# Kernel optimization log

Hardware: AMD Instinct MI355X
Metric: run time of the kernel (lower is better)

The kernel has to match this reference:

```python
import jax, jax.numpy as jnp
import numpy as np

N = 100_000          # nodes
E = 1_600_000        # edges (avg degree 16)
LRELU = 0.01         # default nn.LeakyReLU slope (MLP / bottleneck)
SLOPE = 0.2          # GAT attention slope


def leaky(x, s):
    return jnp.where(x >= 0, x, s * x)


def dense_block(x, convW, gamma, beta):
    # x: [N, C0]; convW: [L, G, Cmax]; each layer: BN -> LeakyReLU -> 1x1 conv -> concat
    for i in range(convW.shape[0]):
        c = x.shape[1]                       # static under trace
        mu = x.mean(axis=0)
        var = x.var(axis=0)                  # biased var, matches torch BN train mode
        xn = (x - mu) * jax.lax.rsqrt(var + 1e-5) * gamma[i, :c] + beta[i, :c]
        xn = leaky(xn, LRELU)
        x = jnp.concatenate([x, xn @ convW[i, :, :c].T], axis=1)  # [N, c+G]
    return x


def gat(x, W, a, b, src, dst):
    # single effective head (torch code shares weight/a across heads -> identical heads)
    h = x @ W                                # [N, F]
    F = W.shape[1]
    # per-edge logit: LeakyReLU([h_dst || h_src] @ a)
    e = leaky(h[dst] @ a[:F] + h[src] @ a[F:], SLOPE)   # [E]
    m = jax.ops.segment_max(e, dst, num_segments=N)
    m = jnp.where(jnp.isfinite(m), m, 0.0)
    ex = jnp.exp(e - m[dst])
    den = jax.ops.segment_sum(ex, dst, num_segments=N)
    alpha = ex / (den[dst] + 1e-16)
    out = jax.ops.segment_sum(alpha[:, None] * h[src], dst, num_segments=N)
    return out + b


def setup_inputs() -> dict:
    key = jax.random.key(0)
    ks = jax.random.split(key, 16)

    def w(k, shape, fan_in):
        return jax.random.normal(k, shape, jnp.float32) / np.float32(np.sqrt(fan_in))

    return {
        "x": jax.random.normal(ks[0], (N, 64), jnp.float32),
        "src": jax.random.randint(ks[1], (E,), 0, N, jnp.int64 if jax.config.jax_enable_x64 else jnp.int32),
        "dst": jax.random.randint(ks[2], (E,), 0, N, jnp.int64 if jax.config.jax_enable_x64 else jnp.int32),
        "mlp_w1": w(ks[3], (64, 256), 64),
        "mlp_b1": jnp.zeros((256,), jnp.float32),
        "mlp_w2": w(ks[4], (256, 256), 256),
        "mlp_b2": jnp.zeros((256,), jnp.float32),
        "mlp_w3": w(ks[5], (256, 24), 256),
        "mlp_b3": jnp.zeros((24,), jnp.float32),
        "conv1": w(ks[6], (6, 12, 84), 84),
        "bn1_g": jnp.ones((6, 84), jnp.float32),
        "bn1_b": jnp.zeros((6, 84), jnp.float32),
        "gat1_w": w(ks[7], (96, 48), 96),
        "gat1_a": jax.random.normal(ks[8], (96,), jnp.float32) * 0.1,
        "gat1_b": jnp.zeros((48,), jnp.float32),
        "conv2": w(ks[9], (6, 12, 108), 108),
        "bn2_g": jnp.ones((6, 108), jnp.float32),
        "bn2_b": jnp.zeros((6, 108), jnp.float32),
        "gat2_w": w(ks[10], (120, 60), 120),
        "gat2_a": jax.random.normal(ks[11], (120,), jnp.float32) * 0.1,
        "gat2_b": jnp.zeros((60,), jnp.float32),
        "conv3": w(ks[12], (6, 12, 120), 120),
        "bn3_g": jnp.ones((6, 120), jnp.float32),
        "bn3_b": jnp.zeros((6, 120), jnp.float32),
    }


def reference(x, src, dst,
              mlp_w1, mlp_b1, mlp_w2, mlp_b2, mlp_w3, mlp_b3,
              conv1, bn1_g, bn1_b, gat1_w, gat1_a, gat1_b,
              conv2, bn2_g, bn2_b, gat2_w, gat2_a, gat2_b,
              conv3, bn3_g, bn3_b):
    h = leaky(x @ mlp_w1 + mlp_b1, LRELU)
    h = leaky(h @ mlp_w2 + mlp_b2, LRELU)
    h = leaky(h @ mlp_w3 + mlp_b3, LRELU)          # [N, 24]
    h = dense_block(h, conv1, bn1_g, bn1_b)        # [N, 96]
    h = gat(h, gat1_w, gat1_a, gat1_b, src, dst)   # [N, 48]
    h = dense_block(h, conv2, bn2_g, bn2_b)        # [N, 120]
    h = gat(h, gat2_w, gat2_a, gat2_b, src, dst)   # [N, 60]
    h = dense_block(h, conv3, bn3_g, bn3_b)        # [N, 132]
    return h
```

## Files before the change

### kernel.cpp

```cpp
#include <hip/hip_runtime.h>
#include <math.h>

#define N_NODES 100000
#define N_EDGES 1600000

static constexpr int GG = (N_NODES + 63) / 64;
static constexpr int NODE_GRID = (N_NODES + 255) / 256;
static constexpr int NB = (N_NODES + 255) / 256;

typedef __attribute__((ext_vector_type(8))) short          bf16x8;
typedef __attribute__((ext_vector_type(8))) unsigned short ushort8_t;
typedef __attribute__((ext_vector_type(4))) unsigned short ushort4_t;
typedef __attribute__((ext_vector_type(4))) float          f32x4;

__device__ __forceinline__ float lrelu(float v, float s){ return v >= 0.f ? v : v*s; }

__device__ __forceinline__ unsigned short f2bf(float f){
    unsigned u = __float_as_uint(f);
    unsigned r = (u + 0x7FFFu + ((u >> 16) & 1u)) >> 16;
    return (unsigned short)r;
}
__device__ __forceinline__ float bf2f(unsigned short h){
    return __uint_as_float(((unsigned)h) << 16);
}

__global__ void cvt_wT_split(const float* __restrict__ w,
                             unsigned short* __restrict__ whi,
                             unsigned short* __restrict__ wlo,
                             int K, int Nsrc, int Npad)
{
    int idx = blockIdx.x * 256 + threadIdx.x;
    if (idx >= Npad * K) return;
    int n = idx / K, k = idx % K;
    float v = (n < Nsrc) ? w[(long)k * Nsrc + n] : 0.f;
    unsigned short hi = f2bf(v);
    whi[idx] = hi;
    wlo[idx] = f2bf(v - bf2f(hi));
}

template<int KV>
__global__ __launch_bounds__(256) void mlp_mfma_hilo(
    const float* __restrict__ A,
    const unsigned short* __restrict__ wth, const unsigned short* __restrict__ wtl,
    const float* __restrict__ bias, float* __restrict__ Out)
{
    constexpr int AS = KV + 8;
    __shared__ unsigned short lds_hi[64 * AS];
    __shared__ unsigned short lds_lo[64 * AS];
    const int t = threadIdx.x;
    const int r0 = blockIdx.x * 64;
    const int wv = t >> 6, lane = t & 63;
    const int l15 = lane & 15, grp = lane >> 4;
    const int cw = wv * 64;

    constexpr int cpr = KV / 8;
    for (int c = t; c < 64 * cpr; c += 256) {
        int row = c / cpr, kc = c % cpr;
        int gr = r0 + row;
        float4 v0 = make_float4(0,0,0,0), v1 = v0;
        if (gr < N_NODES) {
            v0 = *(const float4*)(A + (long)gr * KV + kc * 8);
            v1 = *(const float4*)(A + (long)gr * KV + kc * 8 + 4);
        }
        float vs[8] = {v0.x,v0.y,v0.z,v0.w,v1.x,v1.y,v1.z,v1.w};
        unsigned short* ph = lds_hi + row * AS + kc * 8;
        unsigned short* pl = lds_lo + row * AS + kc * 8;
#pragma unroll
        for (int j = 0; j < 8; j++) {
            unsigned short hi = f2bf(vs[j]);
            ph[j] = hi;
            pl[j] = f2bf(vs[j] - bf2f(hi));
        }
    }
    __syncthreads();

    f32x4 acc[4][4];
#pragma unroll
    for (int i = 0; i < 4; i++)
#pragma unroll
        for (int j = 0; j < 4; j++) acc[i][j] = (f32x4){0.f,0.f,0.f,0.f};

#pragma unroll
    for (int ks = 0; ks < KV / 32; ks++) {
        bf16x8 ah[4], al[4], bh[4], bl[4];
#pragma unroll
        for (int i = 0; i < 4; i++) {
            ah[i] = *(const bf16x8*)(lds_hi + (i*16 + l15) * AS + ks*32 + grp*8);
            al[i] = *(const bf16x8*)(lds_lo + (i*16 + l15) * AS + ks*32 + grp*8);
        }
#pragma unroll
        for (int j = 0; j < 4; j++) {
            bh[j] = *(const bf16x8*)(wth + (size_t)(cw + j*16 + l15) * KV + ks*32 + grp*8);
            bl[j] = *(const bf16x8*)(wtl + (size_t)(cw + j*16 + l15) * KV + ks*32 + grp*8);
        }
#pragma unroll
        for (int i = 0; i < 4; i++)
#pragma unroll
            for (int j = 0; j < 4; j++) {
                acc[i][j] = __builtin_amdgcn_mfma_f32_16x16x32_bf16(ah[i], bl[j], acc[i][j], 0, 0, 0);
                acc[i][j] = __builtin_amdgcn_mfma_f32_16x16x32_bf16(al[i], bh[j], acc[i][j], 0, 0, 0);
                acc[i][j] = __builtin_amdgcn_mfma_f32_16x16x32_bf16(ah[i], bh[j], acc[i][j], 0, 0, 0);
            }
    }

    __syncthreads();
#pragma unroll
    for (int i = 0; i < 4; i++)
#pragma unroll
        for (int j = 0; j < 4; j++)
#pragma unroll
            for (int r = 0; r < 4; r++) {
                int row = r0 + i*16 + grp*4 + r;
                int col = cw + j*16 + l15;
                if (row < N_NODES) {
                    float v = acc[i][j][r] + bias[col];
                    Out[(long)row * 256 + col] = lrelu(v, 0.01f);
                }
            }
}

__global__ __launch_bounds__(256) void mlp_mfma24_hilo(
    const float* __restrict__ A,
    const unsigned short* __restrict__ wth, const unsigned short* __restrict__ wtl,
    const float* __restrict__ bias, float* __restrict__ XtOut)
{
    constexpr int KV = 256, AS = 264;
    __shared__ unsigned short lds_hi[64 * AS];
    __shared__ unsigned short lds_lo[64 * AS];
    const int t = threadIdx.x;
    const int r0 = blockIdx.x * 64;
    const int wv = t >> 6, lane = t & 63;
    const int l15 = lane & 15, grp = lane >> 4;

    constexpr int cpr = KV / 8;
    for (int c = t; c < 64 * cpr; c += 256) {
        int row = c / cpr, kc = c % cpr;
        int gr = r0 + row;
        float4 v0 = make_float4(0,0,0,0), v1 = v0;
        if (gr < N_NODES) {
            v0 = *(const float4*)(A + (long)gr * KV + kc * 8);
            v1 = *(const float4*)(A + (long)gr * KV + kc * 8 + 4);
        }
        float vs[8] = {v0.x,v0.y,v0.z,v0.w,v1.x,v1.y,v1.z,v1.w};
        unsigned short* ph = lds_hi + row * AS + kc * 8;
        unsigned short* pl = lds_lo + row * AS + kc * 8;
#pragma unroll
        for (int j = 0; j < 8; j++) {
            unsigned short hi = f2bf(vs[j]);
            ph[j] = hi;
            pl[j] = f2bf(vs[j] - bf2f(hi));
        }
    }
    __syncthreads();

    f32x4 acc[2] = {(f32x4){0.f,0.f,0.f,0.f}, (f32x4){0.f,0.f,0.f,0.f}};
#pragma unroll
    for (int ks = 0; ks < KV / 32; ks++) {
        bf16x8 ah = *(const bf16x8*)(lds_hi + (wv*16 + l15) * AS + ks*32 + grp*8);
        bf16x8 al = *(const bf16x8*)(lds_lo + (wv*16 + l15) * AS + ks*32 + grp*8);
#pragma unroll
        for (int j = 0; j < 2; j++) {
            bf16x8 bh = *(const bf16x8*)(wth + (size_t)(j*16 + l15) * KV + ks*32 + grp*8);
            bf16x8 bl = *(const bf16x8*)(wtl + (size_t)(j*16 + l15) * KV + ks*32 + grp*8);
            acc[j] = __builtin_amdgcn_mfma_f32_16x16x32_bf16(ah, bl, acc[j], 0, 0, 0);
            acc[j] = __builtin_amdgcn_mfma_f32_16x16x32_bf16(al, bh, acc[j], 0, 0, 0);
            acc[j] = __builtin_amdgcn_mfma_f32_16x16x32_bf16(ah, bh, acc[j], 0, 0, 0);
        }
    }

    __syncthreads();
    float* ldsf = (float*)lds_hi;
#pragma unroll
    for (int j = 0; j < 2; j++)
#pragma unroll
        for (int r = 0; r < 4; r++) {
            int cl = j*16 + l15;
            if (cl < 24) {
                int rl = wv*16 + grp*4 + r;
                float v = acc[j][r] + bias[cl];
                ldsf[rl * 25 + cl] = lrelu(v, 0.01f);
            }
        }
    __syncthreads();
    int n = t & 63, c0 = t >> 6;
    int gr = r0 + n;
    if (gr < N_NODES)
        for (int c = c0; c < 24; c += 4)
            XtOut[(long)c * N_NODES + gr] = ldsf[n * 25 + c];
}

__global__ void bn_stats_t(const float* __restrict__ Xt,
                           float* __restrict__ gsum, float* __restrict__ gsq)
{
    int ch = blockIdx.x, part = blockIdx.y, t = threadIdx.x;
    const float* p = Xt + (long)ch * N_NODES;
    float s = 0.f, q = 0.f;
    for (long i = (long)part * 25000 + t * 4; i < (long)(part + 1) * 25000; i += 1024) {
        float4 v = *(const float4*)(p + i);
        s += v.x + v.y + v.z + v.w;
        q += v.x*v.x + v.y*v.y + v.z*v.z + v.w*v.w;
    }
#pragma unroll
    for (int m = 1; m < 64; m <<= 1) {
        s += __shfl_xor(s, m, 64);
        q += __shfl_xor(q, m, 64);
    }
    __shared__ float ls[4], lq[4];
    int wid = t >> 6;
    if ((t & 63) == 0) { ls[wid] = s; lq[wid] = q; }
    __syncthreads();
    if (t == 0) {
        atomicAdd(gsum + ch, ls[0] + ls[1] + ls[2] + ls[3]);
        atomicAdd(gsq  + ch, lq[0] + lq[1] + lq[2] + lq[3]);
    }
}

__global__ __launch_bounds__(256) void dense_conv2(
    float* __restrict__ Xt, int C, int C0, int layerIdx,
    const float* __restrict__ W, int WS,
    const float* __restrict__ gamma, const float* __restrict__ beta,
    const float* __restrict__ gsum, const float* __restrict__ gsq,
    float* __restrict__ psq)
{
    constexpr int QOFF = 6 * 12 * NB;
    __shared__ float w_lds[12 * 132];
    __shared__ float a_lds[132], b_lds[132];
    __shared__ float red[2][4][12];
    const int t = threadIdx.x;

    for (int c = t; c < C; c += 256) {
        float s, q;
        if (c < C0) { s = gsum[c]; q = gsq[c]; }
        else {
            int lc = c - C0;
            int lj = lc / 12, g = lc % 12;
            const float* pp = psq + ((size_t)lj * 12 + g) * NB;
            const float* qq = pp + QOFF;
            s = 0.f; q = 0.f;
            for (int b = 0; b < NB; b++) { s += pp[b]; q += qq[b]; }
        }
        float mu  = s * (1.f / N_NODES);
        float var = q * (1.f / N_NODES) - mu * mu;
        float A = rsqrtf(var + 1e-5f) * gamma[c];
        a_lds[c] = A;
        b_lds[c] = beta[c] - mu * A;
    }
    for (int i = t; i < 12 * C; i += 256) {
        int g = i / C, c = i - g * C;
        w_lds[g * 132 + c] = W[g * WS + c];
    }
    __syncthreads();

    long n = (long)blockIdx.x * 256 + t;
    bool valid = (n < N_NODES);
    const float* xp = Xt + (valid ? n : 0);
    float acc[12];
#pragma unroll
    for (int g = 0; g < 12; g++) acc[g] = 0.f;

    float v[12], vn[12];
#pragma unroll
    for (int j = 0; j < 12; j++) v[j] = xp[(long)j * N_NODES];
    for (int c0 = 0; c0 < C; c0 += 12) {
        if (c0 + 12 < C) {
#pragma unroll
            for (int j = 0; j < 12; j++)
                vn[j] = xp[(long)(c0 + 12 + j) * N_NODES];
        }
#pragma unroll
        for (int j = 0; j < 12; j++) {
            int ch = c0 + j;
            float u = a_lds[ch] * v[j] + b_lds[ch];
            u = (u >= 0.f) ? u : 0.01f * u;
#pragma unroll
            for (int g = 0; g < 12; g++)
                acc[g] += u * w_lds[g * 132 + ch];
        }
#pragma unroll
        for (int j = 0; j < 12; j++) v[j] = vn[j];
    }
    if (valid) {
#pragma unroll
        for (int g = 0; g < 12; g++)
            Xt[(long)(C + g) * N_NODES + n] = acc[g];
    }

    if (layerIdx < 5) {
        float sv[12], qv[12];
#pragma unroll
        for (int g = 0; g < 12; g++) {
            float a = valid ? acc[g] : 0.f;
            sv[g] = a; qv[g] = a * a;
        }
#pragma unroll
        for (int m = 1; m < 64; m <<= 1)
#pragma unroll
            for (int g = 0; g < 12; g++) {
                sv[g] += __shfl_xor(sv[g], m, 64);
                qv[g] += __shfl_xor(qv[g], m, 64);
            }
        int wid = t >> 6;
        if ((t & 63) == 0) {
#pragma unroll
            for (int g = 0; g < 12; g++) { red[0][wid][g] = sv[g]; red[1][wid][g] = qv[g]; }
        }
        __syncthreads();
        if (t < 12) {
            float s = red[0][0][t] + red[0][1][t] + red[0][2][t] + red[0][3][t];
            float q = red[1][0][t] + red[1][1][t] + red[1][2][t] + red[1][3][t];
            psq[((size_t)layerIdx * 12 + t) * NB + blockIdx.x] = s;
            psq[QOFF + ((size_t)layerIdx * 12 + t) * NB + blockIdx.x] = q;
        }
    }
}

template<int F>
__global__ __launch_bounds__(256) void gat_gemm(
    const float* __restrict__ A, const float* __restrict__ B,
    const float* __restrict__ avec, int K,
    unsigned short* __restrict__ Hb, float* __restrict__ sd, float* __restrict__ ss)
{
    __shared__ float At[16 * 68];
    __shared__ float Bt[16 * 64];
    __shared__ float ad[64], as_[64];
    const int t  = threadIdx.x;
    const int r0 = blockIdx.x * 64;
    const int tx = t & 15, ty = t >> 4;
    if (t < 64) {
        ad[t]  = (t < F) ? avec[t]     : 0.f;
        as_[t] = (t < F) ? avec[F + t] : 0.f;
    }

    float acc[4][4];
#pragma unroll
    for (int i = 0; i < 4; i++)
#pragma unroll
        for (int j = 0; j < 4; j++) acc[i][j] = 0.f;

    for (int k0 = 0; k0 < K; k0 += 16) {
        {
            int kk = t >> 4, rq = t & 15;
            float4 v = make_float4(0.f,0.f,0.f,0.f);
            if (k0 + kk < K)
                v = *(const float4*)(A + (long)(k0 + kk) * N_NODES + r0 + rq * 4);
            *(float4*)(At + kk * 68 + rq * 4) = v;
        }
        for (int i = t; i < 16 * 64; i += 256) {
            int kk = i >> 6, mq = i & 63;
            float v = 0.f;
            if (k0 + kk < K && mq < F) v = B[(long)(k0 + kk) * F + mq];
            Bt[kk * 64 + mq] = v;
        }
        __syncthreads();
#pragma unroll
        for (int kk = 0; kk < 16; kk++) {
            float4 av = *(const float4*)(At + kk * 68 + ty * 4);
            float4 bv = *(const float4*)(Bt + kk * 64 + tx * 4);
            float a_[4] = {av.x, av.y, av.z, av.w};
            float b_[4] = {bv.x, bv.y, bv.z, bv.w};
#pragma unroll
            for (int i = 0; i < 4; i++)
#pragma unroll
                for (int j = 0; j < 4; j++)
                    acc[i][j] += a_[i] * b_[j];
        }
        __syncthreads();
    }

#pragma unroll
    for (int i = 0; i < 4; i++) {
        int row = r0 + ty * 4 + i;
        float pd = 0.f, pq_ = 0.f;
#pragma unroll
        for (int j = 0; j < 4; j++) {
            int col = tx * 4 + j;
            pd  += acc[i][j] * ad[col];
            pq_ += acc[i][j] * as_[col];
        }
#pragma unroll
        for (int m = 1; m < 16; m <<= 1) {
            pd  += __shfl_xor(pd,  m, 64);
            pq_ += __shfl_xor(pq_, m, 64);
        }
        if (row < N_NODES) {
            if (tx == 0) { sd[row] = pd; ss[row] = pq_; }
            if (tx * 4 < F) {
                ushort4_t u;
#pragma unroll
                for (int j = 0; j < 4; j++) u[j] = f2bf(acc[i][j]);
                *(ushort4_t*)(Hb + (long)row * 64 + tx * 4) = u;
            }
        }
    }
}

template<int F>
__global__ __launch_bounds__(256) void gat_aggregate2(
    const int* __restrict__ rstart, const int* __restrict__ csr_src,
    const float* __restrict__ sd, const float* __restrict__ ss,
    const unsigned short* __restrict__ Hb,
    const float* __restrict__ bias, float* __restrict__ outT)
{
    __shared__ float tile[64 * (F + 1)];
    const int t = threadIdx.x;
    const int wid = t >> 6, lane = t & 63;
    const long n0 = (long)blockIdx.x * 64;

#pragma unroll 1
    for (int k = 0; k < 16; k++) {
        long node = n0 + wid * 16 + k;
        float res = 0.f;
        if (node < N_NODES) {
            int st = rstart[node], en = rstart[node + 1];
            int deg = en - st;
            float sdn = sd[node];
            float acc = 0.f, dsum = 0.f;
            if (deg <= 64) {
                int sj = 0; float v = -3.4e38f;
                if (lane < deg) {
                    sj = csr_src[st + lane];
                    v = lrelu(sdn + ss[sj], 0.2f);
                }
                float m = v;
#pragma unroll
                for (int o = 1; o < 64; o <<= 1) m = fmaxf(m, __shfl_xor(m, o, 64));
                float p = (lane < deg) ? __expf(v - m) : 0.f;
                dsum = p;
                int j = 0;
                for (; j + 4 <= deg; j += 4) {
                    float a0 = __shfl(p, j, 64),   a1 = __shfl(p, j+1, 64);
                    float a2 = __shfl(p, j+2, 64), a3 = __shfl(p, j+3, 64);
                    int   s0 = __shfl(sj, j, 64),   s1 = __shfl(sj, j+1, 64);
                    int   s2 = __shfl(sj, j+2, 64), s3 = __shfl(sj, j+3, 64);
                    if (lane < F) {
                        float h0 = bf2f(Hb[(long)s0 * 64 + lane]);
                        float h1 = bf2f(Hb[(long)s1 * 64 + lane]);
                        float h2 = bf2f(Hb[(long)s2 * 64 + lane]);
                        float h3 = bf2f(Hb[(long)s3 * 64 + lane]);
                        acc += a0 * h0; acc += a1 * h1; acc += a2 * h2; acc += a3 * h3;
                    }
                }
                for (; j < deg; j++) {
                    float a = __shfl(p, j, 64);
                    int   s = __shfl(sj, j, 64);
                    if (lane < F) acc += a * bf2f(Hb[(long)s * 64 + lane]);
                }
            } else {
                float m = -3.4e38f;
                for (int base = st; base < en; base += 64) {
                    int cnt = min(64, en - base);
                    float v = -3.4e38f;
                    if (lane < cnt) {
                        int s = csr_src[base + lane];
                        v = lrelu(sdn + ss[s], 0.2f);
                    }
#pragma unroll
                    for (int o = 1; o < 64; o <<= 1) v = fmaxf(v, __shfl_xor(v, o, 64));
                    m = fmaxf(m, v);
                }
                for (int base = st; base < en; base += 64) {
                    int cnt = min(64, en - base);
                    float p = 0.f; int sj = 0;
                    if (lane < cnt) {
                        sj = csr_src[base + lane];
                        float v = lrelu(sdn + ss[sj], 0.2f);
                        p = __expf(v - m);
                    }
                    dsum += p;
                    int j = 0;
                    for (; j + 4 <= cnt; j += 4) {
                        float a0 = __shfl(p, j, 64),   a1 = __shfl(p, j+1, 64);
                        float a2 = __shfl(p, j+2, 64), a3 = __shfl(p, j+3, 64);
                        int   s0 = __shfl(sj, j, 64),   s1 = __shfl(sj, j+1, 64);
                        int   s2 = __shfl(sj, j+2, 64), s3 = __shfl(sj, j+3, 64);
                        if (lane < F) {
                            float h0 = bf2f(Hb[(long)s0 * 64 + lane]);
                            float h1 = bf2f(Hb[(long)s1 * 64 + lane]);
                            float h2 = bf2f(Hb[(long)s2 * 64 + lane]);
                            float h3 = bf2f(Hb[(long)s3 * 64 + lane]);
                            acc += a0 * h0; acc += a1 * h1; acc += a2 * h2; acc += a3 * h3;
                        }
                    }
                    for (; j < cnt; j++) {
                        float a = __shfl(p, j, 64);
                        int   s = __shfl(sj, j, 64);
                        if (lane < F) acc += a * bf2f(Hb[(long)s * 64 + lane]);
                    }
                }
            }
#pragma unroll
            for (int o = 1; o < 64; o <<= 1) dsum += __shfl_xor(dsum, o, 64);
            res = acc / (dsum + 1e-16f);
        }
        if (lane < F) tile[(wid * 16 + k) * (F + 1) + lane] = res + bias[lane];
    }
    __syncthreads();
    for (int idx = t; idx < F * 64; idx += 256) {
        int c = idx / 64, i = idx % 64;
        long n = n0 + i;
        if (n < N_NODES) outT[(long)c * N_NODES + n] = tile[i * (F + 1) + c];
    }
}

__global__ __launch_bounds__(256) void transpose_out(const float* __restrict__ Xt,
                                                     float* __restrict__ out)
{
    __shared__ float tile[64 * 133];
    int t = threadIdx.x;
    long n0 = (long)blockIdx.x * 64;
    int lane = t & 63, cq = t >> 6;
    for (int c = cq; c < 132; c += 4) {
        long n = n0 + lane;
        float v = (n < N_NODES) ? Xt[(long)c * N_NODES + n] : 0.f;
        tile[lane * 133 + c] = v;
    }
    __syncthreads();
    for (int idx = t; idx < 64 * 132; idx += 256) {
        int r = idx / 132, c = idx % 132;
        long n = n0 + r;
        if (n < N_NODES) out[n * 132 + c] = tile[r * 133 + c];
    }
}

__global__ void hist_kernel(const int* __restrict__ dst, int* __restrict__ deg)
{
    for (long e = (long)blockIdx.x * 256 + threadIdx.x; e < N_EDGES; e += (long)gridDim.x * 256)
        atomicAdd(deg + dst[e], 1);
}

__global__ void scan1(const int* __restrict__ deg, int* __restrict__ rtmp, int* __restrict__ parts)
{
    __shared__ int ls[256];
    int t = threadIdx.x;
    long i = (long)blockIdx.x * 256 + t;
    int v = (i < N_NODES) ? deg[i] : 0;
    ls[t] = v; __syncthreads();
    for (int o = 1; o < 256; o <<= 1) {
        int y = (t >= o) ? ls[t - o] : 0;
        __syncthreads();
        ls[t] += y;
        __syncthreads();
    }
    if (i < N_NODES) rtmp[i] = ls[t] - v;
    if (t == 255) parts[blockIdx.x] = ls[255];
}

__global__ void scan2(int* __restrict__ parts, int nb, int* __restrict__ total_out)
{
    __shared__ int ls[512];
    int t = threadIdx.x;
    int v = (t < nb) ? parts[t] : 0;
    ls[t] = v; __syncthreads();
    for (int o = 1; o < 512; o <<= 1) {
        int y = (t >= o) ? ls[t - o] : 0;
        __syncthreads();
        ls[t] += y;
        __syncthreads();
    }
    if (t < nb) parts[t] = ls[t] - v;
    if (t == 0) total_out[0] = ls[511];
}

__global__ void scan3(const int* __restrict__ rtmp, const int* __restrict__ parts,
                      int* __restrict__ rstart, int* __restrict__ cursor)
{
    long i = (long)blockIdx.x * 256 + threadIdx.x;
    if (i < N_NODES) {
        int v = rtmp[i] + parts[i >> 8];
        rstart[i] = v;
        cursor[i] = v;
    }
}

__global__ void scatter_k(const int* __restrict__ src, const int* __restrict__ dst,
                          int* __restrict__ cursor, int* __restrict__ csr_src)
{
    for (long e = (long)blockIdx.x * 256 + threadIdx.x; e < N_EDGES; e += (long)gridDim.x * 256) {
        int pos = atomicAdd(cursor + dst[e], 1);
        csr_src[pos] = src[e];
    }
}

static void run_dense_block_t(hipStream_t stream, float* Xt, int C0,
                              const float* convW, int WS,
                              const float* gamma, const float* beta,
                              float* gsum, float* gsq, float* psq)
{
    hipMemsetAsync(gsum, 0, 264 * sizeof(float), stream);
    bn_stats_t<<<dim3(C0, 4), 256, 0, stream>>>(Xt, gsum, gsq);
    for (int i = 0; i < 6; i++) {
        int C = C0 + 12 * i;
        dense_conv2<<<NB, 256, 0, stream>>>(Xt, C, C0, i, convW + (size_t)i * 12 * WS, WS,
                                            gamma + (size_t)i * WS, beta + (size_t)i * WS,
                                            gsum, gsq, psq);
    }
}

template<int F>
static void run_gat(hipStream_t stream, const float* XtIn, int K,
                    const float* W, const float* avec, const float* bias,
                    unsigned short* Hb, float* outT,
                    float* sd, float* ss, const int* rstart, const int* csr_src)
{
    gat_gemm<F><<<GG, 256, 0, stream>>>(XtIn, W, avec, K, Hb, sd, ss);
    gat_aggregate2<F><<<GG, 256, 0, stream>>>(rstart, csr_src, sd, ss, Hb, bias, outT);
}

extern "C" void kernel_launch(void* const* d_in, const int* in_sizes, int n_in,
                              void* d_out, int out_size, void* d_ws, size_t ws_size,
                              hipStream_t stream)
{
    const float* x     = (const float*)d_in[0];
    const int*   src   = (const int*)d_in[1];
    const int*   dst   = (const int*)d_in[2];
    const float* w1    = (const float*)d_in[3];
    const float* b1    = (const float*)d_in[4];
    const float* w2    = (const float*)d_in[5];
    const float* b2    = (const float*)d_in[6];
    const float* w3    = (const float*)d_in[7];
    const float* b3    = (const float*)d_in[8];
    const float* conv1 = (const float*)d_in[9];
    const float* bn1g  = (const float*)d_in[10];
    const float* bn1b  = (const float*)d_in[11];
    const float* g1w   = (const float*)d_in[12];
    const float* g1a   = (const float*)d_in[13];
    const float* g1b   = (const float*)d_in[14];
    const float* conv2 = (const float*)d_in[15];
    const float* bn2g  = (const float*)d_in[16];
    const float* bn2b  = (const float*)d_in[17];
    const float* g2w   = (const float*)d_in[18];
    const float* g2a   = (const float*)d_in[19];
    const float* g2b   = (const float*)d_in[20];
    const float* conv3 = (const float*)d_in[21];
    const float* bn3g  = (const float*)d_in[22];
    const float* bn3b  = (const float*)d_in[23];
    float* out = (float*)d_out;

    char* ws = (char*)d_ws;
    size_t off = 0;
    auto alloc = [&](size_t bytes) -> void* {
        void* p = ws + off;
        off += (bytes + 255) & ~(size_t)255;
        return p;
    };
    float*    h      = (float*)alloc((size_t)N_NODES * 256 * 4);
    float*    Xt1    = (float*)alloc((size_t)96  * N_NODES * 4);
    float*    Xt2    = (float*)alloc((size_t)120 * N_NODES * 4);
    int*      csr_src= (int*)alloc((size_t)N_EDGES * 4);
    int*      deg    = (int*)alloc((size_t)N_NODES * 4);
    int*      rtmp   = (int*)alloc((size_t)N_NODES * 4);
    int*      rstart = (int*)alloc((size_t)(N_NODES + 1) * 4);
    int*      cursor = (int*)alloc((size_t)N_NODES * 4);
    int*      parts  = (int*)alloc(2048);
    float*    sd     = (float*)alloc((size_t)N_NODES * 4);
    float*    ss     = (float*)alloc((size_t)N_NODES * 4);
    float*    gsum   = (float*)alloc(264 * 4);
    float*    gsq    = gsum + 132;
    float*    psq    = (float*)alloc((size_t)2 * 6 * 12 * NB * 4);
    unsigned short* wt1h = (unsigned short*)alloc(256 * 64  * 2);
    unsigned short* wt1l = (unsigned short*)alloc(256 * 64  * 2);
    unsigned short* wt2h = (unsigned short*)alloc(256 * 256 * 2);
    unsigned short* wt2l = (unsigned short*)alloc(256 * 256 * 2);
    unsigned short* wt3h = (unsigned short*)alloc(32  * 256 * 2);
    unsigned short* wt3l = (unsigned short*)alloc(32  * 256 * 2);

    unsigned short* Hb  = (unsigned short*)h;
    float* Xt3 = (float*)((char*)h + (size_t)16 * 1024 * 1024);

    hipMemsetAsync(deg, 0, (size_t)N_NODES * 4, stream);
    hist_kernel<<<2048, 256, 0, stream>>>(dst, deg);
    scan1<<<NODE_GRID, 256, 0, stream>>>(deg, rtmp, parts);
    scan2<<<1, 512, 0, stream>>>(parts, NODE_GRID, rstart + N_NODES);
    scan3<<<NODE_GRID, 256, 0, stream>>>(rtmp, parts, rstart, cursor);
    scatter_k<<<2048, 256, 0, stream>>>(src, dst, cursor, csr_src);

    cvt_wT_split<<<(256 * 64  + 255) / 256, 256, 0, stream>>>(w1, wt1h, wt1l, 64,  256, 256);
    cvt_wT_split<<<(256 * 256 + 255) / 256, 256, 0, stream>>>(w2, wt2h, wt2l, 256, 256, 256);
    cvt_wT_split<<<(32  * 256 + 255) / 256, 256, 0, stream>>>(w3, wt3h, wt3l, 256, 24,  32);

    mlp_mfma_hilo<64> <<<GG, 256, 0, stream>>>(x, wt1h, wt1l, b1, h);
    mlp_mfma_hilo<256><<<GG, 256, 0, stream>>>(h, wt2h, wt2l, b2, h);
    mlp_mfma24_hilo<<<GG, 256, 0, stream>>>(h, wt3h, wt3l, b3, Xt1);

    run_dense_block_t(stream, Xt1, 24, conv1, 84, bn1g, bn1b, gsum, gsq, psq);

    run_gat<48>(stream, Xt1, 96, g1w, g1a, g1b, Hb, Xt2, sd, ss, rstart, csr_src);

    run_dense_block_t(stream, Xt2, 48, conv2, 108, bn2g, bn2b, gsum, gsq, psq);

    run_gat<60>(stream, Xt2, 120, g2w, g2a, g2b, Hb, Xt3, sd, ss, rstart, csr_src);

    run_dense_block_t(stream, Xt3, 60, conv3, 120, bn3g, bn3b, gsum, gsq, psq);

    transpose_out<<<GG, 256, 0, stream>>>(Xt3, out);
}
```

Before: 1.152 ms.

## Build CSR via two-level bucket sort and wave-parallel BN partial reduction

Replaces the per-node histogram/scan/scatter CSR construction with a bucketed two-pass sort: edges are first binned by dst>>8 using LDS-local histograms and padded bucket counters, then each bucket is locally sorted in shared memory to emit rstart and csr_src. This is meant to cut global atomic contention on 100k per-node counters and the random scatter writes. It also changes the dense_conv2 prologue so each wavefront reduces a channel's per-block BN partials cooperatively with shuffles instead of one thread serially summing all blocks. The cost is an extra 8-byte pairs buffer pass, and edge order within a node becomes nondeterministic, which can alter floating-point summation order.

```diff
diff --git a/kernel.cpp b/kernel.cpp
--- a/kernel.cpp
+++ b/kernel.cpp
@@ -5,8 +5,8 @@
 #define N_EDGES 1600000
 
 static constexpr int GG = (N_NODES + 63) / 64;
-static constexpr int NODE_GRID = (N_NODES + 255) / 256;
 static constexpr int NB = (N_NODES + 255) / 256;
+static constexpr int NBKT = (N_NODES + 255) / 256;
 
 typedef __attribute__((ext_vector_type(8))) short          bf16x8;
 typedef __attribute__((ext_vector_type(8))) unsigned short ushort8_t;
@@ -227,24 +227,35 @@
     __shared__ float a_lds[132], b_lds[132];
     __shared__ float red[2][4][12];
     const int t = threadIdx.x;
-
-    for (int c = t; c < C; c += 256) {
-        float s, q;
-        if (c < C0) { s = gsum[c]; q = gsq[c]; }
-        else {
-            int lc = c - C0;
-            int lj = lc / 12, g = lc % 12;
-            const float* pp = psq + ((size_t)lj * 12 + g) * NB;
-            const float* qq = pp + QOFF;
-            s = 0.f; q = 0.f;
-            for (int b = 0; b < NB; b++) { s += pp[b]; q += qq[b]; }
-        }
+    const int wid = t >> 6, lane = t & 63;
+
+    for (int c = t; c < C0; c += 256) {
+        float s = gsum[c], q = gsq[c];
         float mu  = s * (1.f / N_NODES);
         float var = q * (1.f / N_NODES) - mu * mu;
         float A = rsqrtf(var + 1e-5f) * gamma[c];
         a_lds[c] = A;
         b_lds[c] = beta[c] - mu * A;
     }
+    for (int gc = wid; gc < C - C0; gc += 4) {
+        const float* pp = psq + (size_t)gc * NB;
+        const float* qq = psq + QOFF + (size_t)gc * NB;
+        float s = 0.f, q = 0.f;
+        for (int b = lane; b < NB; b += 64) { s += pp[b]; q += qq[b]; }
+#pragma unroll
+        for (int o = 1; o < 64; o <<= 1) {
+            s += __shfl_xor(s, o, 64);
+            q += __shfl_xor(q, o, 64);
+        }
+        if (lane == 0) {
+            int c = C0 + gc;
+            float mu  = s * (1.f / N_NODES);
+            float var = q * (1.f / N_NODES) - mu * mu;
+            float A = rsqrtf(var + 1e-5f) * gamma[c];
+            a_lds[c] = A;
+            b_lds[c] = beta[c] - mu * A;
+        }
+    }
     for (int i = t; i < 12 * C; i += 256) {
         int g = i / C, c = i - g * C;
         w_lds[g * 132 + c] = W[g * WS + c];
@@ -299,8 +310,7 @@
                 sv[g] += __shfl_xor(sv[g], m, 64);
                 qv[g] += __shfl_xor(qv[g], m, 64);
             }
-        int wid = t >> 6;
-        if ((t & 63) == 0) {
+        if (lane == 0) {
 #pragma unroll
             for (int g = 0; g < 12; g++) { red[0][wid][g] = sv[g]; red[1][wid][g] = qv[g]; }
         }
@@ -522,34 +532,25 @@
     }
 }
 
-__global__ void hist_kernel(const int* __restrict__ dst, int* __restrict__ deg)
-{
+__global__ __launch_bounds__(256) void bkt_hist(const int* __restrict__ dst,
+                                                int* __restrict__ bcnt)
+{
+    __shared__ int lh[NBKT];
+    for (int i = threadIdx.x; i < NBKT; i += 256) lh[i] = 0;
+    __syncthreads();
     for (long e = (long)blockIdx.x * 256 + threadIdx.x; e < N_EDGES; e += (long)gridDim.x * 256)
-        atomicAdd(deg + dst[e], 1);
-}
-
-__global__ void scan1(const int* __restrict__ deg, int* __restrict__ rtmp, int* __restrict__ parts)
-{
-    __shared__ int ls[256];
-    int t = threadIdx.x;
-    long i = (long)blockIdx.x * 256 + t;
-    int v = (i < N_NODES) ? deg[i] : 0;
-    ls[t] = v; __syncthreads();
-    for (int o = 1; o < 256; o <<= 1) {
-        int y = (t >= o) ? ls[t - o] : 0;
-        __syncthreads();
-        ls[t] += y;
-        __syncthreads();
-    }
-    if (i < N_NODES) rtmp[i] = ls[t] - v;
-    if (t == 255) parts[blockIdx.x] = ls[255];
-}
-
-__global__ void scan2(int* __restrict__ parts, int nb, int* __restrict__ total_out)
+        atomicAdd(&lh[dst[e] >> 8], 1);
+    __syncthreads();
+    for (int i = threadIdx.x; i < NBKT; i += 256)
+        if (lh[i]) atomicAdd(&bcnt[i * 16], lh[i]);
+}
+
+__global__ void bkt_scan(const int* __restrict__ bcnt, int* __restrict__ boff,
+                         int* __restrict__ bcur, int* __restrict__ rstart)
 {
     __shared__ int ls[512];
     int t = threadIdx.x;
-    int v = (t < nb) ? parts[t] : 0;
+    int v = (t < NBKT) ? bcnt[t * 16] : 0;
     ls[t] = v; __syncthreads();
     for (int o = 1; o < 512; o <<= 1) {
         int y = (t >= o) ? ls[t - o] : 0;
@@ -557,27 +558,52 @@
         ls[t] += y;
         __syncthreads();
     }
-    if (t < nb) parts[t] = ls[t] - v;
-    if (t == 0) total_out[0] = ls[511];
-}
-
-__global__ void scan3(const int* __restrict__ rtmp, const int* __restrict__ parts,
-                      int* __restrict__ rstart, int* __restrict__ cursor)
-{
-    long i = (long)blockIdx.x * 256 + threadIdx.x;
-    if (i < N_NODES) {
-        int v = rtmp[i] + parts[i >> 8];
-        rstart[i] = v;
-        cursor[i] = v;
-    }
-}
-
-__global__ void scatter_k(const int* __restrict__ src, const int* __restrict__ dst,
-                          int* __restrict__ cursor, int* __restrict__ csr_src)
+    if (t < NBKT) { int ex = ls[t] - v; boff[t] = ex; bcur[t * 16] = ex; }
+    if (t == 0) { boff[NBKT] = N_EDGES; rstart[N_NODES] = N_EDGES; }
+}
+
+__global__ void bkt_scatter(const int* __restrict__ src, const int* __restrict__ dst,
+                            int* __restrict__ bcur, int2* __restrict__ pairs)
 {
     for (long e = (long)blockIdx.x * 256 + threadIdx.x; e < N_EDGES; e += (long)gridDim.x * 256) {
-        int pos = atomicAdd(cursor + dst[e], 1);
-        csr_src[pos] = src[e];
+        int d = dst[e];
+        int pos = atomicAdd(&bcur[(d >> 8) * 16], 1);
+        pairs[pos] = make_int2(d, src[e]);
+    }
+}
+
+__global__ __launch_bounds__(256) void bkt_build(const int2* __restrict__ pairs,
+                                                 const int* __restrict__ boff,
+                                                 int* __restrict__ rstart,
+                                                 int* __restrict__ csr_src)
+{
+    __shared__ int lh[256], sc[256], lbase[256], lcur[256];
+    int b = blockIdx.x, t = threadIdx.x;
+    int st = boff[b], en = boff[b + 1];
+    lh[t] = 0;
+    __syncthreads();
+    for (int i = st + t; i < en; i += 256)
+        atomicAdd(&lh[pairs[i].x & 255], 1);
+    __syncthreads();
+    int v = lh[t];
+    sc[t] = v; __syncthreads();
+    for (int o = 1; o < 256; o <<= 1) {
+        int y = (t >= o) ? sc[t - o] : 0;
+        __syncthreads();
+        sc[t] += y;
+        __syncthreads();
+    }
+    int ex = sc[t] - v;
+    lbase[t] = st + ex;
+    lcur[t] = 0;
+    int node = (b << 8) + t;
+    if (node < N_NODES) rstart[node] = st + ex;
+    __syncthreads();
+    for (int i = st + t; i < en; i += 256) {
+        int2 p = pairs[i];
+        int ld = p.x & 255;
+        int pos = lbase[ld] + atomicAdd(&lcur[ld], 1);
+        csr_src[pos] = p.y;
     }
 }
 
@@ -647,11 +673,11 @@
     float*    Xt1    = (float*)alloc((size_t)96  * N_NODES * 4);
     float*    Xt2    = (float*)alloc((size_t)120 * N_NODES * 4);
     int*      csr_src= (int*)alloc((size_t)N_EDGES * 4);
-    int*      deg    = (int*)alloc((size_t)N_NODES * 4);
-    int*      rtmp   = (int*)alloc((size_t)N_NODES * 4);
+    int2*     pairs  = (int2*)alloc((size_t)N_EDGES * 8);
     int*      rstart = (int*)alloc((size_t)(N_NODES + 1) * 4);
-    int*      cursor = (int*)alloc((size_t)N_NODES * 4);
-    int*      parts  = (int*)alloc(2048);
+    int*      bcnt   = (int*)alloc((size_t)NBKT * 16 * 4);
+    int*      bcur   = (int*)alloc((size_t)NBKT * 16 * 4);
+    int*      boff   = (int*)alloc((size_t)(NBKT + 1) * 4);
     float*    sd     = (float*)alloc((size_t)N_NODES * 4);
     float*    ss     = (float*)alloc((size_t)N_NODES * 4);
     float*    gsum   = (float*)alloc(264 * 4);
@@ -667,12 +693,11 @@
     unsigned short* Hb  = (unsigned short*)h;
     float* Xt3 = (float*)((char*)h + (size_t)16 * 1024 * 1024);
 
-    hipMemsetAsync(deg, 0, (size_t)N_NODES * 4, stream);
-    hist_kernel<<<2048, 256, 0, stream>>>(dst, deg);
-    scan1<<<NODE_GRID, 256, 0, stream>>>(deg, rtmp, parts);
-    scan2<<<1, 512, 0, stream>>>(parts, NODE_GRID, rstart + N_NODES);
-    scan3<<<NODE_GRID, 256, 0, stream>>>(rtmp, parts, rstart, cursor);
-    scatter_k<<<2048, 256, 0, stream>>>(src, dst, cursor, csr_src);
+    hipMemsetAsync(bcnt, 0, (size_t)NBKT * 16 * 4, stream);
+    bkt_hist<<<512, 256, 0, stream>>>(dst, bcnt);
+    bkt_scan<<<1, 512, 0, stream>>>(bcnt, boff, bcur, rstart);
+    bkt_scatter<<<2048, 256, 0, stream>>>(src, dst, bcur, pairs);
+    bkt_build<<<NBKT, 256, 0, stream>>>(pairs, boff, rstart, csr_src);
 
     cvt_wT_split<<<(256 * 64  + 255) / 256, 256, 0, stream>>>(w1, wt1h, wt1l, 64,  256, 256);
     cvt_wT_split<<<(256 * 256 + 255) / 256, 256, 0, stream>>>(w2, wt2h, wt2l, 256, 256, 256);
```

New measurement: 1.190 ms. 3.3% more time.
